# Performance work log

Measured on AMD Instinct MI355X. Metric: run time of the kernel, lower is better.

Reference implementation:

```python
import jax, jax.numpy as jnp
from jax import lax
import numpy as np

N, T, V, C, K, NIN, TSTEPS = 4096, 1, 26, 256, 3, 9, 25


def setup_inputs() -> dict:
    key = jax.random.key(0)
    ks = jax.random.split(key, 28)
    s = 0.02
    inp = {
        "inputs": jax.random.normal(ks[0], (N, T, V * 3), jnp.float32),
        "inputs_previous": jax.random.normal(ks[1], (N, T, V * 3), jnp.float32),
        "inputs_previous2": jax.random.normal(ks[2], (N, T, V * 3), jnp.float32),
        "hidden": jax.random.normal(ks[3], (N, C, V), jnp.float32),
        # graph adjacency buffer [k_num, V, V] (non-trainable) + edge weights
        "A": jax.random.uniform(ks[4], (K, V, V), jnp.float32),
        "emul": jnp.ones((K, V, V), jnp.float32),
        "eadd": jnp.ones((K, V, V), jnp.float32),
        # DecodeGcn conv1d kernel_size=1 -> stored as [C*K, C] matrix
        "conv_w": jax.random.normal(ks[5], (C * K, C), jnp.float32) * s,
        "conv_b": jnp.zeros((C * K,), jnp.float32),
        # GRU input projections (bias=True), Linear(n_in_dec=9 -> C)
        "Wir": jax.random.normal(ks[6], (C, NIN), jnp.float32) * s,
        "bir": jnp.zeros((C,), jnp.float32),
        "Wii": jax.random.normal(ks[7], (C, NIN), jnp.float32) * s,
        "bii": jnp.zeros((C,), jnp.float32),
        "Win": jax.random.normal(ks[8], (C, NIN), jnp.float32) * s,
        "b_in": jnp.zeros((C,), jnp.float32),
        # GRU hidden projections (bias=False)
        "Whr": jax.random.normal(ks[9], (C, C), jnp.float32) * s,
        "Whi": jax.random.normal(ks[10], (C, C), jnp.float32) * s,
        "Whh": jax.random.normal(ks[11], (C, C), jnp.float32) * s,
        # output MLP head
        "W1": jax.random.normal(ks[12], (C, C), jnp.float32) * s,
        "b1": jnp.zeros((C,), jnp.float32),
        "W2": jax.random.normal(ks[13], (C, C), jnp.float32) * s,
        "b2": jnp.zeros((C,), jnp.float32),
        "W3": jax.random.normal(ks[14], (3, C), jnp.float32) * s,
        "b3": jnp.zeros((3,), jnp.float32),
        "t": TSTEPS,
    }
    return inp


def reference(inputs, inputs_previous, inputs_previous2, hidden, A, emul, eadd,
              conv_w, conv_b, Wir, bir, Wii, bii, Win, b_in, Whr, Whi, Whh,
              W1, b1, W2, b2, W3, b3, t):
    n_batch, n_t, d = inputs.shape
    v = A.shape[1]
    k_num = A.shape[0]
    c = hidden.shape[1]

    x0 = inputs.reshape(n_batch, n_t, v, -1)[:, 0]            # [N,V,3]
    xp = inputs_previous.reshape(n_batch, n_t, v, -1)[:, 0]   # [N,V,3]
    xp2 = inputs_previous2.reshape(n_batch, n_t, v, -1)[:, 0]  # [N,V,3]

    A_adj = A * emul + eadd  # [k,V,V]
    # noise injected on position channels each step (torch.randn * 0.0005)
    noise = jax.random.normal(jax.random.key(1), (t, n_batch, v, 3), jnp.float32) * 5e-4

    def gcn(h):  # h: [N,C,V] -> [N,C,V]   (kernel-size-1 conv + graph einsum)
        y = jnp.einsum('ncv,oc->nov', h, conv_w) + conv_b[None, :, None]  # [N,C*k,V]
        y = y.reshape(n_batch, k_num, c, v)
        return jnp.einsum('nkcv,kvw->ncw', y, A_adj)

    def step(carry, inp):
        hid, h1, h2, h3 = carry  # hid: [N,C,V]; h1/h2/h3: last three predictions [N,V,3]
        s, nz = inp
        msg = lax.cond(s < 10, gcn, lambda h: h, hid)  # [N,C,V]
        # unified history recurrence (covers step 0/1/2/>=3 branches):
        ins_p = h1
        ins_v = h2 - h3
        ins_a = ins_p - h2 - ins_v
        x = jnp.concatenate([ins_p + nz, ins_v, ins_a], axis=-1)  # [N,V,9]
        m = msg.transpose(0, 2, 1)       # [N,V,C]
        hprev = hid.transpose(0, 2, 1)   # [N,V,C]
        r = jax.nn.sigmoid(x @ Wir.T + bir + m @ Whr.T)
        z = jax.nn.sigmoid(x @ Wii.T + bii + m @ Whi.T)
        nn_ = jnp.tanh(x @ Win.T + b_in + r * (m @ Whh.T))
        hnew = (1.0 - z) * nn_ + z * hprev  # [N,V,C]
        # output MLP (dropout in eval mode = identity), leaky_relu slope 0.1
        hd = jax.nn.leaky_relu(hnew @ W1.T + b1, 0.1)
        hd = jax.nn.leaky_relu(hd @ W2.T + b2, 0.1)
        res = hd @ W3.T + b3                 # [N,V,3]
        pred = x[:, :, :3] + res             # pred_ = (ins_p + noise) + residual
        return (hnew.transpose(0, 2, 1), pred, h1, h2), pred

    init = (hidden, x0, xp, xp2)
    _, preds = lax.scan(step, init, (jnp.arange(t), noise))  # preds: [t,N,V,3]
    return preds.transpose(1, 2, 0, 3)  # [N,V,t,3] == preds.transpose(1,2) in torch
```

## Files before the change

### kernel.cpp

```cpp
#include <hip/hip_runtime.h>

#define M_ROWS 106496
#define NBATCH 4096
#define VN 26
#define KNUM 3
#define TS 25

typedef unsigned short u16;
typedef __attribute__((ext_vector_type(8))) short v8s;
typedef __attribute__((ext_vector_type(4))) float v4f;

__device__ __forceinline__ u16 f2bf(float f) {
    unsigned u = __float_as_uint(f);
    u += 0x7FFF + ((u >> 16) & 1);
    return (u16)(u >> 16);
}
__device__ __forceinline__ float bf2f(u16 h) {
    return __uint_as_float(((unsigned)h) << 16);
}
__device__ __forceinline__ float sigm(float x) {
    return 1.f / (1.f + __expf(-x));
}
__device__ __forceinline__ float tanh_fast(float x) {
    return 2.f / (1.f + __expf(-2.f * x)) - 1.f;
}

typedef const __attribute__((address_space(1))) unsigned int* gas_t;
typedef __attribute__((address_space(3))) unsigned int* las_t;
__device__ __forceinline__ void gl16(const void* g, void* l) {
    __builtin_amdgcn_global_load_lds((gas_t)g, (las_t)l, 16, 0, 0);
}

template <int ACT>
__global__ __launch_bounds__(256) void gemm_nt(
    const u16* __restrict__ A, const u16* __restrict__ Bt,
    const float* __restrict__ bias, u16* __restrict__ C, int nc)
{
    __shared__ u16 Al[2][128 * 32];
    __shared__ u16 Bl[2][128 * 32];
    const int m0 = blockIdx.x * 128;
    const int n0 = blockIdx.y * 128;
    const int tid = threadIdx.x;
    const int wid = tid >> 6, lane = tid & 63;
    const int ln = lane & 15, q = lane >> 4;
    const int qs8 = (q ^ ((ln >> 1) & 3)) * 8;
    const int wm = (wid >> 1) * 64, wn = (wid & 1) * 64;
    const int srow = tid >> 2;
    const int spart = (tid & 3) ^ ((srow >> 1) & 3);

    const u16* gA0 = &A[(size_t)(m0 + srow) * 256 + spart * 8];
    const u16* gB0 = &Bt[(size_t)(n0 + srow) * 256 + spart * 8];

#define STG(b, kk) do {                                                     \
        gl16(gA0 + (kk) * 32,            &Al[b][wid * 512]);                \
        gl16(gA0 + 64 * 256 + (kk) * 32, &Al[b][2048 + wid * 512]);         \
        gl16(gB0 + (kk) * 32,            &Bl[b][wid * 512]);                \
        gl16(gB0 + 64 * 256 + (kk) * 32, &Bl[b][2048 + wid * 512]);         \
    } while (0)

    v4f acc[4][4] = {};
    STG(0, 0);
    __syncthreads();
#pragma unroll
    for (int kt = 0; kt < 8; ++kt) {
        const int cb = kt & 1, nb = cb ^ 1;
        if (kt < 7) STG(nb, kt + 1);
        v8s af[4], bfv[4];
#pragma unroll
        for (int i = 0; i < 4; ++i)
            af[i] = *(const v8s*)&Al[cb][(wm + i * 16 + ln) * 32 + qs8];
#pragma unroll
        for (int j = 0; j < 4; ++j)
            bfv[j] = *(const v8s*)&Bl[cb][(wn + j * 16 + ln) * 32 + qs8];
#pragma unroll
        for (int i = 0; i < 4; ++i)
#pragma unroll
            for (int j = 0; j < 4; ++j)
                acc[i][j] = __builtin_amdgcn_mfma_f32_16x16x32_bf16(
                    af[i], bfv[j], acc[i][j], 0, 0, 0);
        __syncthreads();
    }
#undef STG
#pragma unroll
    for (int i = 0; i < 4; ++i)
#pragma unroll
        for (int j = 0; j < 4; ++j) {
            int gc = n0 + wn + j * 16 + ln;
            float b = bias[gc];
#pragma unroll
            for (int r = 0; r < 4; ++r) {
                int gr = m0 + wm + i * 16 + q * 4 + r;
                float v = acc[i][j][r] + b;
                if (ACT) v = v > 0.f ? v : 0.1f * v;
                C[(size_t)gr * nc + gc] = f2bf(v);
            }
        }
}

__global__ __launch_bounds__(256) void mlp_head(
    const u16* __restrict__ A, const u16* __restrict__ w1,
    const float* __restrict__ b1, const u16* __restrict__ w2,
    const float* __restrict__ b2, const float* __restrict__ w3,
    const float* __restrict__ b3, const float* __restrict__ p1,
    const float* __restrict__ p2, float* __restrict__ pnew,
    u16* __restrict__ xpad, float* __restrict__ out, int s)
{
    __shared__ u16 Ast[2][64 * 32];
    __shared__ u16 Bst[2][256 * 32];
    __shared__ u16 hdl[64 * 256];
    __shared__ float resl[2][64][3];
    const int m0 = blockIdx.x * 64;
    const int tid = threadIdx.x;
    const int wid = tid >> 6, lane = tid & 63;
    const int ln = lane & 15, q = lane >> 4;
    const int qs8 = (q ^ ((ln >> 1) & 3)) * 8;
    const int wm = (wid >> 1) * 32;
    const int wn = (wid & 1) * 128;
    const int wnh = wid & 1;
    const int srow = tid >> 2;
    const int spart = (tid & 3) ^ ((srow >> 1) & 3);

    const u16* gA0 = &A[(size_t)(m0 + srow) * 256 + spart * 8];
    const u16* gW1 = &w1[(size_t)srow * 256 + spart * 8];
    const u16* gW2 = &w2[(size_t)srow * 256 + spart * 8];

#define STGA(b, kk) gl16(gA0 + (kk) * 32, &Ast[b][wid * 512])
#define STGB(b, kk, W) do {                                                 \
        gl16(W + (kk) * 32,             &Bst[b][wid * 512]);                \
        gl16(W + 64 * 256 + (kk) * 32,  &Bst[b][2048 + wid * 512]);         \
        gl16(W + 128 * 256 + (kk) * 32, &Bst[b][4096 + wid * 512]);         \
        gl16(W + 192 * 256 + (kk) * 32, &Bst[b][6144 + wid * 512]);         \
    } while (0)

    v4f acc[2][8] = {};
    STGA(0, 0); STGB(0, 0, gW1);
    __syncthreads();
    for (int kt = 0; kt < 8; ++kt) {
        const int cb = kt & 1, nb = cb ^ 1;
        if (kt < 7) { STGA(nb, kt + 1); STGB(nb, kt + 1, gW1); }
        else        { STGB(nb, 0, gW2); }
        v8s af[2], bf[8];
#pragma unroll
        for (int i = 0; i < 2; ++i)
            af[i] = *(const v8s*)&Ast[cb][(wm + i * 16 + ln) * 32 + qs8];
#pragma unroll
        for (int j = 0; j < 8; ++j)
            bf[j] = *(const v8s*)&Bst[cb][(wn + j * 16 + ln) * 32 + qs8];
#pragma unroll
        for (int i = 0; i < 2; ++i)
#pragma unroll
            for (int j = 0; j < 8; ++j)
                acc[i][j] = __builtin_amdgcn_mfma_f32_16x16x32_bf16(
                    af[i], bf[j], acc[i][j], 0, 0, 0);
        __syncthreads();
    }

#pragma unroll
    for (int i = 0; i < 2; ++i)
#pragma unroll
        for (int j = 0; j < 8; ++j) {
            int col = wn + j * 16 + ln;
            float bb = b1[col];
#pragma unroll
            for (int r = 0; r < 4; ++r) {
                int row = wm + i * 16 + q * 4 + r;
                float v = acc[i][j][r] + bb;
                v = v > 0.f ? v : 0.1f * v;
                int ch = (col >> 3) ^ (row & 15);
                hdl[row * 256 + ch * 8 + (col & 7)] = f2bf(v);
            }
        }
    __syncthreads();

    v4f acc2[2][8] = {};
    for (int kt = 0; kt < 8; ++kt) {
        const int cb = kt & 1, nb = cb ^ 1;
        if (kt < 7) STGB(nb, kt + 1, gW2);
        v8s af[2], bf[8];
#pragma unroll
        for (int i = 0; i < 2; ++i) {
            int row = wm + i * 16 + ln;
            int ch = (kt * 4 + q) ^ (row & 15);
            af[i] = *(const v8s*)&hdl[row * 256 + ch * 8];
        }
#pragma unroll
        for (int j = 0; j < 8; ++j)
            bf[j] = *(const v8s*)&Bst[cb][(wn + j * 16 + ln) * 32 + qs8];
#pragma unroll
        for (int i = 0; i < 2; ++i)
#pragma unroll
            for (int j = 0; j < 8; ++j)
                acc2[i][j] = __builtin_amdgcn_mfma_f32_16x16x32_bf16(
                    af[i], bf[j], acc2[i][j], 0, 0, 0);
        __syncthreads();
    }
#undef STGA
#undef STGB

    float part[3][2][4] = {};
#pragma unroll
    for (int j = 0; j < 8; ++j) {
        int col = wn + j * 16 + ln;
        float bb = b2[col];
        float w30 = w3[col], w31 = w3[256 + col], w32 = w3[512 + col];
#pragma unroll
        for (int i = 0; i < 2; ++i)
#pragma unroll
            for (int r = 0; r < 4; ++r) {
                float v = acc2[i][j][r] + bb;
                v = v > 0.f ? v : 0.1f * v;
                part[0][i][r] += v * w30;
                part[1][i][r] += v * w31;
                part[2][i][r] += v * w32;
            }
    }
#pragma unroll
    for (int off = 1; off < 16; off <<= 1)
#pragma unroll
        for (int t = 0; t < 3; ++t)
#pragma unroll
            for (int i = 0; i < 2; ++i)
#pragma unroll
                for (int r = 0; r < 4; ++r)
                    part[t][i][r] += __shfl_xor(part[t][i][r], off, 16);
    if (ln == 0) {
#pragma unroll
        for (int i = 0; i < 2; ++i)
#pragma unroll
            for (int r = 0; r < 4; ++r) {
                int row = wm + i * 16 + q * 4 + r;
#pragma unroll
                for (int t = 0; t < 3; ++t)
                    resl[wnh][row][t] = part[t][i][r];
            }
    }
    __syncthreads();

    if (tid < 64) {
        int m = m0 + tid;
        float s0 = resl[0][tid][0] + resl[1][tid][0];
        float s1 = resl[0][tid][1] + resl[1][tid][1];
        float s2 = resl[0][tid][2] + resl[1][tid][2];
        float a0 = p1[m * 3 + 0], a1 = p1[m * 3 + 1], a2 = p1[m * 3 + 2];
        float c0 = p2[m * 3 + 0], c1 = p2[m * 3 + 1], c2 = p2[m * 3 + 2];
        float o0 = a0 + s0 + b3[0];
        float o1 = a1 + s1 + b3[1];
        float o2 = a2 + s2 + b3[2];
        size_t ob = ((size_t)m * TS + s) * 3;
        out[ob + 0] = o0; out[ob + 1] = o1; out[ob + 2] = o2;
        pnew[m * 3 + 0] = o0; pnew[m * 3 + 1] = o1; pnew[m * 3 + 2] = o2;
        unsigned t[32];
#pragma unroll
        for (int i = 0; i < 32; ++i) t[i] = 0;
        t[0] = f2bf(o0); t[1] = f2bf(o1); t[2] = f2bf(o2);
        t[3] = f2bf(a0 - c0); t[4] = f2bf(a1 - c1); t[5] = f2bf(a2 - c2);
        t[6] = f2bf(o0 - 2.f * a0 + c0);
        t[7] = f2bf(o1 - 2.f * a1 + c1);
        t[8] = f2bf(o2 - 2.f * a2 + c2);
        t[9] = f2bf(1.f);
        uint4* dst = (uint4*)&xpad[(size_t)m * 32];
#pragma unroll
        for (int wq = 0; wq < 4; ++wq) {
            uint4 u;
            u.x = t[wq * 8 + 0] | (t[wq * 8 + 1] << 16);
            u.y = t[wq * 8 + 2] | (t[wq * 8 + 3] << 16);
            u.z = t[wq * 8 + 4] | (t[wq * 8 + 5] << 16);
            u.w = t[wq * 8 + 6] | (t[wq * 8 + 7] << 16);
            dst[wq] = u;
        }
    }
}

__global__ __launch_bounds__(256) void graph_mix(
    const u16* __restrict__ y, const float* __restrict__ aadj,
    u16* __restrict__ msg)
{
    __shared__ u16 yl[VN * 768];
    const int n = blockIdx.x, tid = threadIdx.x;
    const uint4* src = (const uint4*)(y + (size_t)n * VN * 768);
    for (int idx = tid; idx < VN * 768 / 8; idx += 256)
        ((uint4*)yl)[idx] = src[idx];
    __syncthreads();
    const int c = tid;
    float acc[VN] = {};
    for (int k = 0; k < KNUM; ++k)
        for (int v = 0; v < VN; ++v) {
            float yv = bf2f(yl[v * 768 + k * 256 + c]);
            const float* ap = &aadj[(k * VN + v) * VN];
#pragma unroll
            for (int w = 0; w < VN; ++w) acc[w] += yv * ap[w];
        }
    size_t base = (size_t)n * VN * 256;
    for (int w = 0; w < VN; ++w) msg[base + w * 256 + c] = f2bf(acc[w]);
}

__global__ __launch_bounds__(256) void gru_fused(
    const u16* __restrict__ Am, const u16* __restrict__ xpad,
    const u16* __restrict__ hprev, u16* __restrict__ hout,
    const u16* __restrict__ wfull, const u16* __restrict__ wxn)
{
    __shared__ u16 Al[128 * 32];
    __shared__ u16 Bl[192 * 32];
    __shared__ u16 Xl[64 * 32];
    const int m0 = blockIdx.x * 128;
    const int n0 = blockIdx.y * 64;
    const int tid = threadIdx.x;
    const int wid = tid >> 6, lane = tid & 63;
    const int ln = lane & 15, q = lane >> 4;
    const int qs8 = (q ^ ((ln >> 1) & 3)) * 8;
    const int wm = (wid >> 1) * 64, wn = (wid & 1) * 32;
    const int srow = tid >> 2;
    const int spart = (tid & 3) ^ ((srow >> 1) & 3);

    gl16(&wxn[(size_t)(n0 + srow) * 32 + spart * 8], &Xl[(wid * 64) * 8]);

    v4f accr[4][2] = {}, accz[4][2] = {}, acch[4][2] = {}, accn[4][2] = {};

    for (int kt = 0; kt < 9; ++kt) {
#pragma unroll
        for (int p = 0; p < 2; ++p) {
            const u16* ga = (kt < 8)
                ? &Am[(size_t)(m0 + p * 64 + srow) * 256 + kt * 32 + spart * 8]
                : &xpad[(size_t)(m0 + p * 64 + srow) * 32 + spart * 8];
            gl16(ga, &Al[(p * 256 + wid * 64) * 8]);
        }
#pragma unroll
        for (int p = 0; p < 3; ++p)
            gl16(&wfull[(size_t)(p * 256 + n0 + srow) * 288 + kt * 32 + spart * 8],
                 &Bl[(p * 256 + wid * 64) * 8]);
        __syncthreads();

        v8s af[4];
#pragma unroll
        for (int i = 0; i < 4; ++i)
            af[i] = *(const v8s*)&Al[(wm + i * 16 + ln) * 32 + qs8];
        v8s bfr[3][2];
#pragma unroll
        for (int g = 0; g < 3; ++g)
#pragma unroll
            for (int j = 0; j < 2; ++j)
                bfr[g][j] = *(const v8s*)&Bl[(g * 64 + wn + j * 16 + ln) * 32 + qs8];
#pragma unroll
        for (int i = 0; i < 4; ++i)
#pragma unroll
            for (int j = 0; j < 2; ++j) {
                accr[i][j] = __builtin_amdgcn_mfma_f32_16x16x32_bf16(af[i], bfr[0][j], accr[i][j], 0, 0, 0);
                accz[i][j] = __builtin_amdgcn_mfma_f32_16x16x32_bf16(af[i], bfr[1][j], accz[i][j], 0, 0, 0);
                acch[i][j] = __builtin_amdgcn_mfma_f32_16x16x32_bf16(af[i], bfr[2][j], acch[i][j], 0, 0, 0);
            }
        if (kt == 8) {
            v8s bfn[2];
#pragma unroll
            for (int j = 0; j < 2; ++j)
                bfn[j] = *(const v8s*)&Xl[(wn + j * 16 + ln) * 32 + qs8];
#pragma unroll
            for (int i = 0; i < 4; ++i)
#pragma unroll
                for (int j = 0; j < 2; ++j)
                    accn[i][j] = __builtin_amdgcn_mfma_f32_16x16x32_bf16(af[i], bfn[j], accn[i][j], 0, 0, 0);
        }
        __syncthreads();
    }

#pragma unroll
    for (int i = 0; i < 4; ++i)
#pragma unroll
        for (int j = 0; j < 2; ++j) {
            int gc = n0 + wn + j * 16 + ln;
#pragma unroll
            for (int r = 0; r < 4; ++r) {
                int gr = m0 + wm + i * 16 + q * 4 + r;
                float rg = sigm(accr[i][j][r]);
                float zg = sigm(accz[i][j][r]);
                float nn = tanh_fast(accn[i][j][r] + rg * acch[i][j][r]);
                float hp = bf2f(hprev[(size_t)gr * 256 + gc]);
                hout[(size_t)gr * 256 + gc] = f2bf((1.f - zg) * nn + zg * hp);
            }
        }
}

__global__ __launch_bounds__(256) void init_xpad(
    const float* __restrict__ x0, const float* __restrict__ xp,
    const float* __restrict__ xp2, u16* __restrict__ xpad)
{
    int m = blockIdx.x * 256 + threadIdx.x;
    float a0 = x0[m * 3 + 0], a1 = x0[m * 3 + 1], a2 = x0[m * 3 + 2];
    float b0 = xp[m * 3 + 0], b1 = xp[m * 3 + 1], b2 = xp[m * 3 + 2];
    float c0 = xp2[m * 3 + 0], c1 = xp2[m * 3 + 1], c2 = xp2[m * 3 + 2];
    unsigned t[32];
#pragma unroll
    for (int i = 0; i < 32; ++i) t[i] = 0;
    t[0] = f2bf(a0); t[1] = f2bf(a1); t[2] = f2bf(a2);
    t[3] = f2bf(b0 - c0); t[4] = f2bf(b1 - c1); t[5] = f2bf(b2 - c2);
    t[6] = f2bf(a0 - 2.f * b0 + c0);
    t[7] = f2bf(a1 - 2.f * b1 + c1);
    t[8] = f2bf(a2 - 2.f * b2 + c2);
    t[9] = f2bf(1.f);
    uint4* dst = (uint4*)&xpad[(size_t)m * 32];
#pragma unroll
    for (int wq = 0; wq < 4; ++wq) {
        uint4 u;
        u.x = t[wq * 8 + 0] | (t[wq * 8 + 1] << 16);
        u.y = t[wq * 8 + 2] | (t[wq * 8 + 3] << 16);
        u.z = t[wq * 8 + 4] | (t[wq * 8 + 5] << 16);
        u.w = t[wq * 8 + 6] | (t[wq * 8 + 7] << 16);
        dst[wq] = u;
    }
}

__global__ __launch_bounds__(256) void transpose_h(
    const float* __restrict__ hidden, u16* __restrict__ hA)
{
    __shared__ float hl[256 * VN];
    const int n = blockIdx.x, tid = threadIdx.x;
    const uint4* src = (const uint4*)(hidden + (size_t)n * 256 * VN);
    for (int idx = tid; idx < 256 * VN / 4; idx += 256)
        ((uint4*)hl)[idx] = src[idx];
    __syncthreads();
    size_t base = (size_t)n * VN * 256;
    for (int idx = tid; idx < VN * 256; idx += 256) {
        int v = idx >> 8, c = idx & 255;
        hA[base + idx] = f2bf(hl[c * VN + v]);
    }
}

__global__ __launch_bounds__(256) void pack_weights(
    const float* __restrict__ Whr, const float* __restrict__ Whi,
    const float* __restrict__ Whh, const float* __restrict__ convw_f,
    const float* __restrict__ W1f, const float* __restrict__ W2f,
    const float* __restrict__ Af, const float* __restrict__ emul,
    const float* __restrict__ eadd, const float* __restrict__ Wir,
    const float* __restrict__ Wii, const float* __restrict__ Win,
    const float* __restrict__ bir, const float* __restrict__ bii,
    const float* __restrict__ b_in, const float* __restrict__ convb_f,
    const float* __restrict__ b1f, const float* __restrict__ b2f,
    const float* __restrict__ W3f, const float* __restrict__ b3f,
    u16* __restrict__ wfull, u16* __restrict__ wxn, u16* __restrict__ convw,
    u16* __restrict__ w1, u16* __restrict__ w2, float* __restrict__ aadj,
    float* __restrict__ convb, float* __restrict__ b1, float* __restrict__ b2,
    float* __restrict__ w3, float* __restrict__ b3)
{
    int gid = blockIdx.x * 256 + threadIdx.x;
    int stride = gridDim.x * 256;
    for (int i = gid; i < 768 * 288; i += stride) {
        int row = i / 288, col = i - row * 288;
        int g = row >> 8, c = row & 255;
        float v = 0.f;
        if (col < 256)
            v = (g == 0 ? Whr : (g == 1 ? Whi : Whh))[c * 256 + col];
        else if (col < 265) {
            int tcol = col - 256;
            v = (g == 0 ? Wir[c * 9 + tcol] : (g == 1 ? Wii[c * 9 + tcol] : 0.f));
        } else if (col == 265)
            v = (g == 0 ? bir[c] : (g == 1 ? bii[c] : 0.f));
        wfull[i] = f2bf(v);
    }
    for (int i = gid; i < 256 * 32; i += stride) {
        int c = i >> 5, col = i & 31;
        float v = 0.f;
        if (col < 9) v = Win[c * 9 + col];
        else if (col == 9) v = b_in[c];
        wxn[i] = f2bf(v);
    }
    for (int i = gid; i < 65536; i += stride) {
        w1[i] = f2bf(W1f[i]);
        w2[i] = f2bf(W2f[i]);
    }
    for (int i = gid; i < 196608; i += stride) convw[i] = f2bf(convw_f[i]);
    for (int i = gid; i < KNUM * VN * VN; i += stride)
        aadj[i] = Af[i] * emul[i] + eadd[i];
    for (int i = gid; i < 256; i += stride) { b1[i] = b1f[i]; b2[i] = b2f[i]; }
    for (int i = gid; i < 768; i += stride) { convb[i] = convb_f[i]; w3[i] = W3f[i]; }
    if (gid < 3) b3[gid] = b3f[gid];
}

extern "C" void kernel_launch(void* const* d_in, const int* in_sizes, int n_in,
                              void* d_out, int out_size, void* d_ws, size_t ws_size,
                              hipStream_t stream)
{
    const float* inputs   = (const float*)d_in[0];
    const float* inputs_p = (const float*)d_in[1];
    const float* inputs_p2= (const float*)d_in[2];
    const float* hidden   = (const float*)d_in[3];
    const float* Af       = (const float*)d_in[4];
    const float* emul     = (const float*)d_in[5];
    const float* eadd     = (const float*)d_in[6];
    const float* conv_w   = (const float*)d_in[7];
    const float* conv_b   = (const float*)d_in[8];
    const float* Wir      = (const float*)d_in[9];
    const float* bir      = (const float*)d_in[10];
    const float* Wii      = (const float*)d_in[11];
    const float* bii      = (const float*)d_in[12];
    const float* Win      = (const float*)d_in[13];
    const float* b_in     = (const float*)d_in[14];
    const float* Whr      = (const float*)d_in[15];
    const float* Whi      = (const float*)d_in[16];
    const float* Whh      = (const float*)d_in[17];
    const float* W1f      = (const float*)d_in[18];
    const float* b1f      = (const float*)d_in[19];
    const float* W2f      = (const float*)d_in[20];
    const float* b2f      = (const float*)d_in[21];
    const float* W3f      = (const float*)d_in[22];
    const float* b3f      = (const float*)d_in[23];
    float* out = (float*)d_out;

    const size_t M = M_ROWS;
    char* ws = (char*)d_ws;
    size_t off = 0;
    auto alloc = [&](size_t bytes) -> void* {
        void* p = ws + off;
        off = (off + bytes + 255) & ~(size_t)255;
        return p;
    };
    u16* hA    = (u16*)alloc(M * 256 * 2);
    u16* hB    = (u16*)alloc(M * 256 * 2);
    u16* msg   = (u16*)alloc(M * 256 * 2);
    u16* ybuf  = (u16*)alloc(M * 768 * 2);
    u16* xpad  = (u16*)alloc(M * 32 * 2);
    float* pa  = (float*)alloc(M * 3 * 4);
    float* pb  = (float*)alloc(M * 3 * 4);
    float* pc  = (float*)alloc(M * 3 * 4);
    u16* wfull = (u16*)alloc(768 * 288 * 2);
    u16* wxn   = (u16*)alloc(256 * 32 * 2);
    u16* convw = (u16*)alloc(196608 * 2);
    u16* w1    = (u16*)alloc(65536 * 2);
    u16* w2    = (u16*)alloc(65536 * 2);
    float* aadj  = (float*)alloc(KNUM * VN * VN * 4);
    float* convb = (float*)alloc(768 * 4);
    float* b1    = (float*)alloc(256 * 4);
    float* b2    = (float*)alloc(256 * 4);
    float* w3    = (float*)alloc(768 * 4);
    float* b3    = (float*)alloc(16);
    if (off > ws_size) return;

    pack_weights<<<512, 256, 0, stream>>>(
        Whr, Whi, Whh, conv_w, W1f, W2f, Af, emul, eadd, Wir, Wii, Win,
        bir, bii, b_in, conv_b, b1f, b2f, W3f, b3f,
        wfull, wxn, convw, w1, w2, aadj, convb, b1, b2, w3, b3);
    transpose_h<<<NBATCH, 256, 0, stream>>>(hidden, hA);
    init_xpad<<<M_ROWS / 256, 256, 0, stream>>>(inputs, inputs_p, inputs_p2, xpad);
    hipMemcpyAsync(pa, inputs,    M * 3 * 4, hipMemcpyDeviceToDevice, stream);
    hipMemcpyAsync(pb, inputs_p,  M * 3 * 4, hipMemcpyDeviceToDevice, stream);
    hipMemcpyAsync(pc, inputs_p2, M * 3 * 4, hipMemcpyDeviceToDevice, stream);

    u16* hcur = hA;  u16* hnext = hB;
    float* P1 = pa;  float* P2 = pb;  float* P3 = pc;
    const int MB = M_ROWS / 128;

    for (int s = 0; s < TS; ++s) {
        const u16* m_ptr;
        if (s < 10) {
            gemm_nt<0><<<dim3(MB, 6), 256, 0, stream>>>(hcur, convw, convb, ybuf, 768);
            graph_mix<<<NBATCH, 256, 0, stream>>>(ybuf, aadj, msg);
            m_ptr = msg;
        } else {
            m_ptr = hcur;
        }
        gru_fused<<<dim3(MB, 4), 256, 0, stream>>>(m_ptr, xpad, hcur, hnext,
                                                   wfull, wxn);
        mlp_head<<<M_ROWS / 64, 256, 0, stream>>>(hnext, w1, b1, w2, b2, w3, b3,
                                                  P1, P2, P3, xpad, out, s);
        float* t = P3; P3 = P2; P2 = P1; P1 = t;
        u16* ht = hcur; hcur = hnext; hnext = ht;
    }
}
```

Baseline: 6.020 ms.

## Fuse conv GEMM and graph mixing into one per-batch kernel

Replaces the separate conv1d GEMM and graph_mix kernels with a single conv_mix kernel, one block per batch element. The block computes the 26x768 conv output in LDS with MFMA, then applies the adjacency mixing from LDS. This removes the global write and read-back of the large intermediate ybuf on each of the first ten steps. In exchange, every block re-streams the full conv weight matrix without double buffering. It pads 26 rows to 32, which wastes some MFMA work, and its large LDS footprint limits occupancy.

New measurement: 5.914 ms. About the same (-1.8%).

```diff
diff --git a/kernel.cpp b/kernel.cpp
--- a/kernel.cpp
+++ b/kernel.cpp
@@ -31,70 +31,98 @@
     __builtin_amdgcn_global_load_lds((gas_t)g, (las_t)l, 16, 0, 0);
 }
 
-template <int ACT>
-__global__ __launch_bounds__(256) void gemm_nt(
-    const u16* __restrict__ A, const u16* __restrict__ Bt,
-    const float* __restrict__ bias, u16* __restrict__ C, int nc)
-{
-    __shared__ u16 Al[2][128 * 32];
-    __shared__ u16 Bl[2][128 * 32];
-    const int m0 = blockIdx.x * 128;
-    const int n0 = blockIdx.y * 128;
-    const int tid = threadIdx.x;
+__global__ __launch_bounds__(256) void conv_mix(
+    const u16* __restrict__ h, const u16* __restrict__ convw,
+    const float* __restrict__ convb, const float* __restrict__ aadj,
+    u16* __restrict__ msg)
+{
+    __shared__ u16 Hl[32 * 256];
+    __shared__ u16 Yl[26 * 768];
+    __shared__ u16 Bst[384 * 32];
+    const int n = blockIdx.x, tid = threadIdx.x;
     const int wid = tid >> 6, lane = tid & 63;
     const int ln = lane & 15, q = lane >> 4;
     const int qs8 = (q ^ ((ln >> 1) & 3)) * 8;
-    const int wm = (wid >> 1) * 64, wn = (wid & 1) * 64;
+    const int wn = wid * 96;
     const int srow = tid >> 2;
     const int spart = (tid & 3) ^ ((srow >> 1) & 3);
 
-    const u16* gA0 = &A[(size_t)(m0 + srow) * 256 + spart * 8];
-    const u16* gB0 = &Bt[(size_t)(n0 + srow) * 256 + spart * 8];
-
-#define STG(b, kk) do {                                                     \
-        gl16(gA0 + (kk) * 32,            &Al[b][wid * 512]);                \
-        gl16(gA0 + 64 * 256 + (kk) * 32, &Al[b][2048 + wid * 512]);         \
-        gl16(gB0 + (kk) * 32,            &Bl[b][wid * 512]);                \
-        gl16(gB0 + 64 * 256 + (kk) * 32, &Bl[b][2048 + wid * 512]);         \
-    } while (0)
-
-    v4f acc[4][4] = {};
-    STG(0, 0);
+    for (int idx = tid; idx < 26 * 32; idx += 256) {
+        int row = idx >> 5, g = idx & 31;
+        uint4 v = *(const uint4*)&h[((size_t)n * 26 + row) * 256 + g * 8];
+        int gs = (g & ~3) | ((g & 3) ^ ((row >> 1) & 3));
+        *(uint4*)&Hl[row * 256 + gs * 8] = v;
+    }
+    {
+        uint4 z = {0, 0, 0, 0};
+        for (int idx = tid; idx < 6 * 32; idx += 256) {
+            int row = 26 + (idx >> 5), g = idx & 31;
+            *(uint4*)&Hl[row * 256 + g * 8] = z;
+        }
+    }
+
+    const u16* gW0 = &convw[(size_t)srow * 256 + spart * 8];
+    for (int p = 0; p < 2; ++p) {
+        v4f acc[2][6] = {};
+        const u16* gW = gW0 + (size_t)p * 384 * 256;
+        for (int kt = 0; kt < 8; ++kt) {
+#pragma unroll
+            for (int t = 0; t < 6; ++t)
+                gl16(gW + (size_t)t * 64 * 256 + kt * 32,
+                     &Bst[t * 2048 + wid * 512]);
+            __syncthreads();
+            v8s af[2], bf[6];
+#pragma unroll
+            for (int i = 0; i < 2; ++i)
+                af[i] = *(const v8s*)&Hl[(i * 16 + ln) * 256 + kt * 32 + qs8];
+#pragma unroll
+            for (int j = 0; j < 6; ++j)
+                bf[j] = *(const v8s*)&Bst[(wn + j * 16 + ln) * 32 + qs8];
+#pragma unroll
+            for (int i = 0; i < 2; ++i)
+#pragma unroll
+                for (int j = 0; j < 6; ++j)
+                    acc[i][j] = __builtin_amdgcn_mfma_f32_16x16x32_bf16(
+                        af[i], bf[j], acc[i][j], 0, 0, 0);
+            __syncthreads();
+        }
+#pragma unroll
+        for (int i = 0; i < 2; ++i)
+#pragma unroll
+            for (int j = 0; j < 6; ++j) {
+                int o = p * 384 + wn + j * 16 + ln;
+                float cb = convb[o];
+#pragma unroll
+                for (int r = 0; r < 4; ++r) {
+                    int row = i * 16 + q * 4 + r;
+                    if (row < 26) {
+                        float v = acc[i][j][r] + cb;
+                        int ch = (o >> 3) ^ (row & 7);
+                        Yl[row * 768 + ch * 8 + (o & 7)] = f2bf(v);
+                    }
+                }
+            }
+    }
     __syncthreads();
-#pragma unroll
-    for (int kt = 0; kt < 8; ++kt) {
-        const int cb = kt & 1, nb = cb ^ 1;
-        if (kt < 7) STG(nb, kt + 1);
-        v8s af[4], bfv[4];
-#pragma unroll
-        for (int i = 0; i < 4; ++i)
-            af[i] = *(const v8s*)&Al[cb][(wm + i * 16 + ln) * 32 + qs8];
-#pragma unroll
-        for (int j = 0; j < 4; ++j)
-            bfv[j] = *(const v8s*)&Bl[cb][(wn + j * 16 + ln) * 32 + qs8];
-#pragma unroll
-        for (int i = 0; i < 4; ++i)
-#pragma unroll
-            for (int j = 0; j < 4; ++j)
-                acc[i][j] = __builtin_amdgcn_mfma_f32_16x16x32_bf16(
-                    af[i], bfv[j], acc[i][j], 0, 0, 0);
-        __syncthreads();
-    }
-#undef STG
-#pragma unroll
-    for (int i = 0; i < 4; ++i)
-#pragma unroll
-        for (int j = 0; j < 4; ++j) {
-            int gc = n0 + wn + j * 16 + ln;
-            float b = bias[gc];
-#pragma unroll
-            for (int r = 0; r < 4; ++r) {
-                int gr = m0 + wm + i * 16 + q * 4 + r;
-                float v = acc[i][j][r] + b;
-                if (ACT) v = v > 0.f ? v : 0.1f * v;
-                C[(size_t)gr * nc + gc] = f2bf(v);
-            }
-        }
+    float* aadjl = (float*)Bst;
+    for (int idx = tid; idx < KNUM * VN * VN; idx += 256) aadjl[idx] = aadj[idx];
+    __syncthreads();
+
+    const int c = tid;
+    float accm[VN];
+#pragma unroll
+    for (int w = 0; w < VN; ++w) accm[w] = 0.f;
+    for (int k = 0; k < KNUM; ++k)
+        for (int v = 0; v < VN; ++v) {
+            int o = k * 256 + c;
+            float yv = bf2f(Yl[v * 768 + ((o >> 3) ^ (v & 7)) * 8 + (o & 7)]);
+            const float* ap = &aadjl[(k * VN + v) * VN];
+#pragma unroll
+            for (int w = 0; w < VN; ++w) accm[w] += yv * ap[w];
+        }
+    size_t base = (size_t)n * VN * 256;
+#pragma unroll
+    for (int w = 0; w < VN; ++w) msg[base + w * 256 + c] = f2bf(accm[w]);
 }
 
 __global__ __launch_bounds__(256) void mlp_head(
@@ -269,29 +297,6 @@
             dst[wq] = u;
         }
     }
-}
-
-__global__ __launch_bounds__(256) void graph_mix(
-    const u16* __restrict__ y, const float* __restrict__ aadj,
-    u16* __restrict__ msg)
-{
-    __shared__ u16 yl[VN * 768];
-    const int n = blockIdx.x, tid = threadIdx.x;
-    const uint4* src = (const uint4*)(y + (size_t)n * VN * 768);
-    for (int idx = tid; idx < VN * 768 / 8; idx += 256)
-        ((uint4*)yl)[idx] = src[idx];
-    __syncthreads();
-    const int c = tid;
-    float acc[VN] = {};
-    for (int k = 0; k < KNUM; ++k)
-        for (int v = 0; v < VN; ++v) {
-            float yv = bf2f(yl[v * 768 + k * 256 + c]);
-            const float* ap = &aadj[(k * VN + v) * VN];
-#pragma unroll
-            for (int w = 0; w < VN; ++w) acc[w] += yv * ap[w];
-        }
-    size_t base = (size_t)n * VN * 256;
-    for (int w = 0; w < VN; ++w) msg[base + w * 256 + c] = f2bf(acc[w]);
 }
 
 __global__ __launch_bounds__(256) void gru_fused(
@@ -531,6 +536,7 @@
     float* b2    = (float*)alloc(256 * 4);
     float* w3    = (float*)alloc(768 * 4);
     float* b3    = (float*)alloc(16);
+    (void)ybuf;
     if (off > ws_size) return;
 
     pack_weights<<<512, 256, 0, stream>>>(
@@ -550,8 +556,7 @@
     for (int s = 0; s < TS; ++s) {
         const u16* m_ptr;
         if (s < 10) {
-            gemm_nt<0><<<dim3(MB, 6), 256, 0, stream>>>(hcur, convw, convb, ybuf, 768);
-            graph_mix<<<NBATCH, 256, 0, stream>>>(ybuf, aadj, msg);
+            conv_mix<<<NBATCH, 256, 0, stream>>>(hcur, convw, convb, aadj, msg);
             m_ptr = msg;
         } else {
             m_ptr = hcur;
```
